# Optimization experiments

Measured on AMD Instinct MI355X. Metric: run time of the kernel, lower is better.

The kernel has to match this reference:

```python
import jax, jax.numpy as jnp
import numpy as np

N = 50000
E = 800000
IN_DIM, HID, OUT = 64, 256, 128


def gcn_conv(x, edge_index, W, b):
    """PyG GCNConv with add_self_loops=False, sym normalization, unit edge weights.
    Transform-then-propagate: out[i] = sum_{e: col[e]=i} norm[e] * (x @ W)[row[e]] + b
    norm[e] = deg^-1/2[row] * deg^-1/2[col], deg = in-degree at col.
    """
    n = x.shape[0]
    row, col = edge_index[0], edge_index[1]
    xw = x @ W  # [N, out]
    deg = jax.ops.segment_sum(jnp.ones(row.shape[0], dtype=x.dtype), col, num_segments=n)
    dis = jnp.where(deg > 0, jax.lax.rsqrt(jnp.where(deg > 0, deg, 1.0)), 0.0)
    norm = dis[row] * dis[col]  # [E]
    msg = xw[row] * norm[:, None]  # [E, out]
    out = jax.ops.segment_sum(msg, col, num_segments=n)
    return out + b


def setup_inputs() -> dict:
    key = jax.random.key(0)
    ks = jax.random.split(key, 16)
    def lin(k, fi, fo):
        s = 1.0 / np.sqrt(fi)
        k1, k2 = jax.random.split(k)
        return (jax.random.uniform(k1, (fi, fo), jnp.float32, -s, s),
                jax.random.uniform(k2, (fo,), jnp.float32, -s, s))
    x = jax.random.normal(ks[0], (N, IN_DIM), jnp.float32)
    edge_index = jax.random.randint(ks[1], (2, E), 0, N, dtype=jnp.int64)
    w_fc, b_fc = lin(ks[2], IN_DIM, HID)
    w_conv1, b_conv1 = lin(ks[3], IN_DIM, HID)
    w_fc1, b_fc1 = lin(ks[4], 2 * HID, OUT)
    w_conv2, b_conv2 = lin(ks[5], 2 * HID, OUT)
    w_fc2, b_fc2 = lin(ks[6], OUT, 1)
    w_conv3, b_conv3 = lin(ks[7], OUT, 1)
    return dict(x=x, edge_index=edge_index,
                w_fc=w_fc, b_fc=b_fc, w_conv1=w_conv1, b_conv1=b_conv1,
                w_fc1=w_fc1, b_fc1=b_fc1, w_conv2=w_conv2, b_conv2=b_conv2,
                w_fc2=w_fc2, b_fc2=b_fc2, w_conv3=w_conv3, b_conv3=b_conv3)


def reference(x, edge_index, w_fc, b_fc, w_conv1, b_conv1, w_fc1, b_fc1,
              w_conv2, b_conv2, w_fc2, b_fc2, w_conv3, b_conv3):
    # MTGCL gcn_mlp, eval mode (dropout / dropout_adj are identity)
    x1 = jax.nn.relu(x @ w_fc + b_fc)                       # [N, HID]
    x2 = jax.nn.relu(gcn_conv(x, edge_index, w_conv1, b_conv1))  # [N, HID]
    x3 = jnp.concatenate((x1, x2), axis=1)                  # [N, 2*HID]
    x5 = jax.nn.relu(x3 @ w_fc1 + b_fc1)                    # [N, OUT]
    x6 = jax.nn.relu(gcn_conv(x3, edge_index, w_conv2, b_conv2))
    x7 = x5 + x6                                            # [N, OUT]
    pre = (x7 @ w_fc2 + b_fc2) + gcn_conv(x7, edge_index, w_conv3, b_conv3)
    return pre  # [N, 1]
```

## Files before the change

kernel.cpp:

```cpp
#include <hip/hip_runtime.h>
#include <hip/hip_bf16.h>

typedef __attribute__((ext_vector_type(8))) short short8;
typedef __attribute__((ext_vector_type(4))) float f32x4;

__device__ __forceinline__ ushort bf16_bits(float v) {
    __hip_bfloat16 h = __float2bfloat16(v);
    return *reinterpret_cast<ushort*>(&h);
}
__device__ __forceinline__ float bf16_val(float v) {
    __hip_bfloat16 h = __float2bfloat16(v);
    return __bfloat162float(h);
}
__device__ __forceinline__ float bfu_lo(uint u) {
    uint t = u << 16; return __uint_as_float(t);
}
__device__ __forceinline__ float bfu_hi(uint u) {
    uint t = u & 0xffff0000u; return __uint_as_float(t);
}


__global__ __launch_bounds__(256) void k_bcount(const int* __restrict__ col,
                                                int* __restrict__ bcnt, int E) {
    __shared__ int hist[196];
    int tid = threadIdx.x;
    int base = blockIdx.x * 2048;
    if (tid < 196) hist[tid] = 0;
    __syncthreads();
    #pragma unroll
    for (int i = 0; i < 8; i++) {
        int e = base + i * 256 + tid;
        if (e < E) atomicAdd(&hist[col[e] >> 8], 1);
    }
    __syncthreads();
    if (tid < 196 && hist[tid] > 0) atomicAdd(&bcnt[tid], hist[tid]);
}

__global__ __launch_bounds__(256) void k_bscan(const int* __restrict__ bcnt,
                                               int* __restrict__ bbase,
                                               int* __restrict__ bcur, int E) {
    int i = threadIdx.x;
    int v = (i < 196) ? bcnt[i] : 0;
    int lane = i & 63, w = i >> 6;
    int s = v;
    #pragma unroll
    for (int o = 1; o < 64; o <<= 1) {
        int t = __shfl_up(s, o);
        if (lane >= o) s += t;
    }
    __shared__ int wsum[4];
    if (lane == 63) wsum[w] = s;
    __syncthreads();
    int add = 0;
    for (int ww = 0; ww < w; ww++) add += wsum[ww];
    int excl = s + add - v;
    if (i < 196) {
        bbase[i] = excl;
        bcur[i] = excl;
    }
    if (i == 195) bbase[196] = excl + v;
}

__global__ __launch_bounds__(256) void k_binA(const int* __restrict__ row,
                                              const int* __restrict__ col,
                                              int* __restrict__ bcur,
                                              uint* __restrict__ stage, int E) {
    __shared__ uint colbuf[2048];
    __shared__ int hist[196];
    __shared__ int lcur[196];
    int tid = threadIdx.x;
    int base = blockIdx.x * 2048;
    if (tid < 196) hist[tid] = 0;
    __syncthreads();
    #pragma unroll
    for (int i = 0; i < 8; i++) {
        int e = base + i * 256 + tid;
        uint c = 0xFFFFFFFFu;
        if (e < E) {
            c = (uint)col[e];
            atomicAdd(&hist[c >> 8], 1);
        }
        colbuf[i * 256 + tid] = c;
    }
    __syncthreads();
    if (tid < 196 && hist[tid] > 0) lcur[tid] = atomicAdd(&bcur[tid], hist[tid]);
    __syncthreads();
    #pragma unroll
    for (int i = 0; i < 8; i++) {
        int idx = i * 256 + tid;
        uint c = colbuf[idx];
        if (c != 0xFFFFFFFFu) {
            uint r = (uint)row[base + idx];
            int p = atomicAdd(&lcur[c >> 8], 1);
            stage[p] = (c << 16) | r;
        }
    }
}

__global__ __launch_bounds__(256) void k_binB(const uint* __restrict__ stage,
                                              const int* __restrict__ bbase,
                                              int* __restrict__ rowptr,
                                              float* __restrict__ dis,
                                              ushort* __restrict__ csr16,
                                              int n, int E) {
    __shared__ int cnt[256];
    __shared__ int cur[256];
    __shared__ int wsum[4];
    int b = blockIdx.x;
    int lo = b << 8;
    int tid = threadIdx.x;
    int gstart = bbase[b], gend = bbase[b + 1];
    cnt[tid] = 0;
    __syncthreads();
    for (int idx = gstart + tid; idx < gend; idx += 256)
        atomicAdd(&cnt[(stage[idx] >> 16) & 255], 1);
    __syncthreads();
    int v = cnt[tid];
    int lane = tid & 63, w = tid >> 6;
    int s = v;
    #pragma unroll
    for (int o = 1; o < 64; o <<= 1) {
        int t = __shfl_up(s, o);
        if (lane >= o) s += t;
    }
    if (lane == 63) wsum[w] = s;
    __syncthreads();
    int add = 0;
    for (int ww = 0; ww < w; ww++) add += wsum[ww];
    int excl = s + add - v + gstart;
    int node = lo + tid;
    if (node < n) {
        rowptr[node] = excl;
        dis[node] = v > 0 ? rsqrtf((float)v) : 0.f;
    }
    cur[tid] = excl;
    if (tid == 0 && b == gridDim.x - 1) rowptr[n] = E;
    __syncthreads();
    for (int idx = gstart + tid; idx < gend; idx += 256) {
        uint pk = stage[idx];
        int p = atomicAdd(&cur[(pk >> 16) & 255], 1);
        csr16[p] = (ushort)(pk & 0xffffu);
    }
}


__global__ __launch_bounds__(256) void k_prepX(const float* __restrict__ x,
                                               const float* __restrict__ dis,
                                               ushort* __restrict__ xh,
                                               ushort* __restrict__ xs, int total4) {
    int i = blockIdx.x * 256 + threadIdx.x;
    if (i >= total4) return;
    float4 v = reinterpret_cast<const float4*>(x)[i];
    float dn = dis[i >> 4];
    float vv[4] = {v.x, v.y, v.z, v.w};
    uint hv[2], sv[2];
    #pragma unroll
    for (int g = 0; g < 2; g++) {
        float a0 = vv[g * 2], a1 = vv[g * 2 + 1];
        hv[g] = (uint)bf16_bits(a0) | ((uint)bf16_bits(a1) << 16);
        sv[g] = (uint)bf16_bits(a0 * dn) | ((uint)bf16_bits(a1 * dn) << 16);
    }
    reinterpret_cast<uint2*>(xh)[i] = make_uint2(hv[0], hv[1]);
    reinterpret_cast<uint2*>(xs)[i] = make_uint2(sv[0], sv[1]);
}


__global__ __launch_bounds__(256) void k_agg64_csr(const ushort* __restrict__ xs,
                                                   const int* __restrict__ rowptr,
                                                   const ushort* __restrict__ csr16,
                                                   const float* __restrict__ dis,
                                                   ushort* __restrict__ agghi, int n) {
    int node = blockIdx.x * 4 + (threadIdx.x >> 6);
    if (node >= n) return;
    int lane = threadIdx.x & 63;
    int sub = lane >> 3;
    int li  = lane & 7;
    int s = rowptr[node], t = rowptr[node + 1];
    float acc[8] = {};
    int p = s;
    for (; p + 16 <= t; p += 16) {
        int rr[2];
        #pragma unroll
        for (int u = 0; u < 2; u++) rr[u] = csr16[p + u * 8 + sub];
        uint4 v[2];
        #pragma unroll
        for (int u = 0; u < 2; u++)
            v[u] = *reinterpret_cast<const uint4*>(&xs[(size_t)rr[u] * 64 + li * 8]);
        #pragma unroll
        for (int u = 0; u < 2; u++) {
            acc[0] += bfu_lo(v[u].x); acc[1] += bfu_hi(v[u].x);
            acc[2] += bfu_lo(v[u].y); acc[3] += bfu_hi(v[u].y);
            acc[4] += bfu_lo(v[u].z); acc[5] += bfu_hi(v[u].z);
            acc[6] += bfu_lo(v[u].w); acc[7] += bfu_hi(v[u].w);
        }
    }
    for (; p < t; p += 8) {
        int e = p + sub;
        if (e < t) {
            int rr = csr16[e];
            uint4 v = *reinterpret_cast<const uint4*>(&xs[(size_t)rr * 64 + li * 8]);
            acc[0] += bfu_lo(v.x); acc[1] += bfu_hi(v.x);
            acc[2] += bfu_lo(v.y); acc[3] += bfu_hi(v.y);
            acc[4] += bfu_lo(v.z); acc[5] += bfu_hi(v.z);
            acc[6] += bfu_lo(v.w); acc[7] += bfu_hi(v.w);
        }
    }
    #pragma unroll
    for (int j = 0; j < 8; j++) {
        acc[j] += __shfl_xor(acc[j], 8);
        acc[j] += __shfl_xor(acc[j], 16);
        acc[j] += __shfl_xor(acc[j], 32);
    }
    if (sub == 0) {
        float dn = dis[node];
        uint hp[4];
        #pragma unroll
        for (int g = 0; g < 4; g++) {
            float a0 = acc[g * 2] * dn, a1 = acc[g * 2 + 1] * dn;
            hp[g] = (uint)bf16_bits(a0) | ((uint)bf16_bits(a1) << 16);
        }
        *reinterpret_cast<uint4*>(&agghi[(size_t)node * 64 + li * 8]) =
            make_uint4(hp[0], hp[1], hp[2], hp[3]);
    }
}

__global__ __launch_bounds__(256) void k_agg128_x7dot(
    const ushort* __restrict__ xw,
    const int* __restrict__ rowptr,
    const ushort* __restrict__ csr16,
    const float* __restrict__ dis,
    const float* __restrict__ b2,
    const ushort* __restrict__ x5,
    const float* __restrict__ wfc2, const float* __restrict__ bfc2,
    const float* __restrict__ wc3,  const float* __restrict__ bc3,
    float* __restrict__ out, float* __restrict__ xw3, int n) {
    int node = blockIdx.x * 4 + (threadIdx.x >> 6);
    if (node >= n) return;
    int lane = threadIdx.x & 63;
    int sub = lane >> 4;
    int li  = lane & 15;
    int s = rowptr[node], t = rowptr[node + 1];
    float acc[8] = {};
    int p = s;
    for (; p + 16 <= t; p += 16) {
        int rr[4];
        #pragma unroll
        for (int u = 0; u < 4; u++) rr[u] = csr16[p + u * 4 + sub];
        uint4 v[4];
        #pragma unroll
        for (int u = 0; u < 4; u++)
            v[u] = *reinterpret_cast<const uint4*>(&xw[(size_t)rr[u] * 128 + li * 8]);
        #pragma unroll
        for (int u = 0; u < 4; u++) {
            acc[0] += bfu_lo(v[u].x); acc[1] += bfu_hi(v[u].x);
            acc[2] += bfu_lo(v[u].y); acc[3] += bfu_hi(v[u].y);
            acc[4] += bfu_lo(v[u].z); acc[5] += bfu_hi(v[u].z);
            acc[6] += bfu_lo(v[u].w); acc[7] += bfu_hi(v[u].w);
        }
    }
    for (; p < t; p += 4) {
        int e = p + sub;
        if (e < t) {
            int rr = csr16[e];
            uint4 v = *reinterpret_cast<const uint4*>(&xw[(size_t)rr * 128 + li * 8]);
            acc[0] += bfu_lo(v.x); acc[1] += bfu_hi(v.x);
            acc[2] += bfu_lo(v.y); acc[3] += bfu_hi(v.y);
            acc[4] += bfu_lo(v.z); acc[5] += bfu_hi(v.z);
            acc[6] += bfu_lo(v.w); acc[7] += bfu_hi(v.w);
        }
    }
    #pragma unroll
    for (int j = 0; j < 8; j++) {
        acc[j] += __shfl_xor(acc[j], 16);
        acc[j] += __shfl_xor(acc[j], 32);
    }
    float dn = dis[node];
    float s1 = 0.f, s2 = 0.f;
    if (sub == 0) {
        uint4 xv = *reinterpret_cast<const uint4*>(&x5[(size_t)node * 128 + li * 8]);
        float xr[8] = {bfu_lo(xv.x), bfu_hi(xv.x), bfu_lo(xv.y), bfu_hi(xv.y),
                       bfu_lo(xv.z), bfu_hi(xv.z), bfu_lo(xv.w), bfu_hi(xv.w)};
        #pragma unroll
        for (int j = 0; j < 8; j++) {
            int d = li * 8 + j;
            float x7 = xr[j] + fmaxf(dn * acc[j] + b2[d], 0.f);
            s1 += x7 * wfc2[d];
            s2 += x7 * wc3[d];
        }
    }
    #pragma unroll
    for (int o = 32; o > 0; o >>= 1) {
        s1 += __shfl_down(s1, o);
        s2 += __shfl_down(s2, o);
    }
    if (lane == 0) {
        out[node] = s1 + bfc2[0] + bc3[0];
        xw3[node] = s2 * dn;
    }
}

__global__ __launch_bounds__(256) void k_agg1_csr(const float* __restrict__ sv,
                                                  const int* __restrict__ rowptr,
                                                  const ushort* __restrict__ csr16,
                                                  const float* __restrict__ dis,
                                                  float* __restrict__ out, int n) {
    int i = blockIdx.x * 256 + threadIdx.x;
    if (i >= n) return;
    int s = rowptr[i], t = rowptr[i + 1];
    float a = 0.f;
    #pragma unroll 4
    for (int p = s; p < t; ++p) a += sv[csr16[p]];
    out[i] += dis[i] * a;
}

__global__ __launch_bounds__(256) void k_prepW(const float* __restrict__ w0,
                                               const float* __restrict__ w1,
                                               const float* __restrict__ wf1,
                                               const float* __restrict__ wf2,
                                               ushort* __restrict__ W0f,
                                               ushort* __restrict__ W1f,
                                               ushort* __restrict__ Bf) {
    int id = blockIdx.x * 256 + threadIdx.x;
    if (id < 8192) {
        int mat = id >> 12;
        int rem = id & 4095;
        int lane = rem & 63;
        int nt = (rem >> 6) & 15;
        int k0i = (rem >> 10) & 1;
        int arr = rem >> 11;
        const float* w = mat ? w1 : w0;
        ushort* dst = mat ? W1f : W0f;
        int n = nt * 16 + (lane & 15);
        int kb = k0i * 32 + (lane >> 4) * 8;
        ushort o[8];
        #pragma unroll
        for (int j = 0; j < 8; j++) {
            float v = w[(size_t)(kb + j) * 256 + n];
            o[j] = arr ? bf16_bits(v - bf16_val(v)) : bf16_bits(v);
        }
        *reinterpret_cast<int4*>(&dst[(size_t)rem * 8]) = *reinterpret_cast<const int4*>(o);
    } else if (id < 24576) {
        int rem = id - 8192;
        int lane = rem & 63;
        int nt   = (rem >> 6) & 15;
        int k0i  = (rem >> 10) & 15;
        int n = nt * 16 + (lane & 15);
        int kbase = k0i * 32 + (lane >> 4) * 8;
        ushort outv[8];
        #pragma unroll
        for (int j = 0; j < 8; j++) {
            int k = kbase + j;
            float v = (n < 128) ? wf1[(size_t)k * 128 + n]
                                : wf2[(size_t)k * 128 + (n - 128)];
            outv[j] = bf16_bits(v);
        }
        *reinterpret_cast<int4*>(&Bf[(size_t)rem * 8]) = *reinterpret_cast<const int4*>(outv);
    }
}

__device__ __forceinline__ int x3_swz(int inner) {
    return inner ^ ((((inner >> 6) & 1) << 4) ^ (((inner >> 7) & 1) << 3));
}

__global__ __launch_bounds__(256) void k_mmfused(
    const ushort* __restrict__ xh, const ushort* __restrict__ ah_,
    const ushort* __restrict__ W0f, const ushort* __restrict__ W1f,
    const float* __restrict__ b0, const float* __restrict__ b1,
    const ushort* __restrict__ Bf, const float* __restrict__ bias1,
    const float* __restrict__ dis,
    ushort* __restrict__ C1, ushort* __restrict__ C2, int M) {
    __shared__ ushort x3[4 * 16 * 512];

    const int t = threadIdx.x;
    const int lane = t & 63;
    const int wv = t >> 6;
    const int m0 = blockIdx.x * 64;
    const int ln15 = lane & 15;
    const int quad = lane >> 4;

    f32x4 acc[4][4];

    #pragma unroll
    for (int layer = 0; layer < 2; layer++) {
        const ushort* A = layer ? ah_ : xh;
        const ushort* Wf = layer ? W1f : W0f;
        const float* bias = layer ? b1 : b0;
        #pragma unroll
        for (int mt = 0; mt < 4; mt++)
            #pragma unroll
            for (int nt4 = 0; nt4 < 4; nt4++)
                acc[mt][nt4] = (f32x4){0.f, 0.f, 0.f, 0.f};

        #pragma unroll
        for (int k0i = 0; k0i < 2; k0i++) {
            short8 bh[4], bl[4];
            #pragma unroll
            for (int nt4 = 0; nt4 < 4; nt4++) {
                const ushort* pw = Wf + ((size_t)k0i * 16 + wv * 4 + nt4) * 512 + (size_t)lane * 8;
                bh[nt4] = *reinterpret_cast<const short8*>(pw);
                bl[nt4] = *reinterpret_cast<const short8*>(pw + 16384);
            }
            #pragma unroll
            for (int mt = 0; mt < 4; mt++) {
                int gm = m0 + mt * 16 + ln15;
                int gmc = gm < M - 1 ? gm : M - 1;
                size_t ia = (size_t)gmc * 64 + k0i * 32 + quad * 8;
                short8 a = *reinterpret_cast<const short8*>(&A[ia]);
                #pragma unroll
                for (int nt4 = 0; nt4 < 4; nt4++) {
                    acc[mt][nt4] = __builtin_amdgcn_mfma_f32_16x16x32_bf16(a, bh[nt4], acc[mt][nt4], 0, 0, 0);
                    acc[mt][nt4] = __builtin_amdgcn_mfma_f32_16x16x32_bf16(a, bl[nt4], acc[mt][nt4], 0, 0, 0);
                }
            }
        }

        #pragma unroll
        for (int mt = 0; mt < 4; mt++) {
            #pragma unroll
            for (int nt4 = 0; nt4 < 4; nt4++) {
                int gn = wv * 64 + nt4 * 16 + ln15;
                int gcol = gn + layer * 256;
                int k0f = gcol >> 5, qf = (gcol >> 3) & 3, j = gcol & 7;
                #pragma unroll
                for (int r = 0; r < 4; r++) {
                    int rloc = quad * 4 + r;
                    float v = fmaxf(acc[mt][nt4][r] + bias[gn], 0.f);
                    int inner = x3_swz((qf * 16 + rloc) * 8 + j);
                    x3[(mt * 16 + k0f) * 512 + inner] = bf16_bits(v);
                }
            }
        }
    }
    __syncthreads();

    #pragma unroll
    for (int mt = 0; mt < 4; mt++)
        #pragma unroll
        for (int nt = 0; nt < 4; nt++)
            acc[mt][nt] = (f32x4){0.f, 0.f, 0.f, 0.f};

    const int innerA = x3_swz(lane * 8);
    const ushort* bPtr = Bf + ((size_t)wv * 4) * 512 + (size_t)lane * 8;

    short8 bC[4];
    #pragma unroll
    for (int nt = 0; nt < 4; nt++)
        bC[nt] = *reinterpret_cast<const short8*>(bPtr + (size_t)nt * 512);

    for (int k0 = 0; k0 < 16; k0++) {
        short8 bN[4];
        if (k0 < 15) {
            #pragma unroll
            for (int nt = 0; nt < 4; nt++)
                bN[nt] = *reinterpret_cast<const short8*>(bPtr + ((size_t)(k0 + 1) * 16 + nt) * 512);
        }
        short8 aF[4];
        #pragma unroll
        for (int mt = 0; mt < 4; mt++)
            aF[mt] = *reinterpret_cast<const short8*>(&x3[(mt * 16 + k0) * 512 + innerA]);
        #pragma unroll
        for (int mt = 0; mt < 4; mt++)
            #pragma unroll
            for (int nt = 0; nt < 4; nt++)
                acc[mt][nt] = __builtin_amdgcn_mfma_f32_16x16x32_bf16(aF[mt], bC[nt], acc[mt][nt], 0, 0, 0);
        if (k0 < 15) {
            #pragma unroll
            for (int nt = 0; nt < 4; nt++) bC[nt] = bN[nt];
        }
    }

    #pragma unroll
    for (int mt = 0; mt < 4; mt++) {
        float dn[4];
        #pragma unroll
        for (int r = 0; r < 4; r++) {
            int gm = m0 + mt * 16 + quad * 4 + r;
            dn[r] = (gm < M) ? dis[gm] : 0.f;
        }
        #pragma unroll
        for (int nt = 0; nt < 4; nt++) {
            int gn = wv * 64 + nt * 16 + ln15;
            #pragma unroll
            for (int r = 0; r < 4; r++) {
                int gm = m0 + mt * 16 + quad * 4 + r;
                if (gm >= M) continue;
                float v = acc[mt][nt][r];
                if (gn < 128) {
                    C1[(size_t)gm * 128 + gn] = bf16_bits(fmaxf(v + bias1[gn], 0.f));
                } else {
                    C2[(size_t)gm * 128 + (gn - 128)] = bf16_bits(v * dn[r]);
                }
            }
        }
    }
}

extern "C" void kernel_launch(void* const* d_in, const int* in_sizes, int n_in,
                              void* d_out, int out_size, void* d_ws, size_t ws_size,
                              hipStream_t stream) {
    const float* x       = (const float*)d_in[0];
    const int*   ei      = (const int*)d_in[1];
    const float* w_fc    = (const float*)d_in[2];
    const float* b_fc    = (const float*)d_in[3];
    const float* w_conv1 = (const float*)d_in[4];
    const float* b_conv1 = (const float*)d_in[5];
    const float* w_fc1   = (const float*)d_in[6];
    const float* b_fc1   = (const float*)d_in[7];
    const float* w_conv2 = (const float*)d_in[8];
    const float* b_conv2 = (const float*)d_in[9];
    const float* w_fc2   = (const float*)d_in[10];
    const float* b_fc2   = (const float*)d_in[11];
    const float* w_conv3 = (const float*)d_in[12];
    const float* b_conv3 = (const float*)d_in[13];

    const int N = in_sizes[0] / 64;
    const int E = in_sizes[1] / 2;
    const int* row = ei;
    const int* col = ei + E;

    const int nb = (N + 255) / 256;
    const int nblk = (N + 63) / 64;

    char* p = (char*)d_ws;
    auto alloc = [&](size_t elems) {
        void* q = p; p += ((elems + 3) & ~(size_t)3) * 4; return q;
    };
    int*    bcnt    = (int*)   alloc(200);
    int*    bbase   = (int*)   alloc(200);
    int*    bcur    = (int*)   alloc(200);
    int*    rowptr  = (int*)   alloc(N + 4);
    uint*   stage   = (uint*)  alloc(E);
    ushort* csr16   = (ushort*)alloc((size_t)E / 2);
    float*  dis     = (float*) alloc(N);
    ushort* xh      = (ushort*)alloc((size_t)N * 32);
    ushort* xs      = (ushort*)alloc((size_t)N * 32);
    ushort* agghi   = (ushort*)alloc((size_t)N * 32);
    ushort* Bf      = (ushort*)alloc(65536);
    ushort* W0f     = (ushort*)alloc(16384);
    ushort* W1f     = (ushort*)alloc(16384);
    ushort* x5      = (ushort*)alloc((size_t)N * 64);
    ushort* xw2     = (ushort*)alloc((size_t)N * 64);
    float*  xw3     = (float*) alloc(N);

    float* out = (float*)d_out;

    hipMemsetAsync(bcnt, 0, 196 * sizeof(int), stream);
    k_bcount<<<(E + 2047) / 2048, 256, 0, stream>>>(col, bcnt, E);
    k_bscan<<<1, 256, 0, stream>>>(bcnt, bbase, bcur, E);
    k_binA<<<(E + 2047) / 2048, 256, 0, stream>>>(row, col, bcur, stage, E);
    k_binB<<<nb, 256, 0, stream>>>(stage, bbase, rowptr, dis, csr16, N, E);

    k_prepX<<<(N * 16 + 255) / 256, 256, 0, stream>>>(x, dis, xh, xs, N * 16);
    k_prepW<<<24576 / 256, 256, 0, stream>>>(w_fc, w_conv1, w_fc1, w_conv2,
                                             W0f, W1f, Bf);

    k_agg64_csr<<<(N + 3) / 4, 256, 0, stream>>>(xs, rowptr, csr16, dis, agghi, N);

    k_mmfused<<<nblk, 256, 0, stream>>>(xh, agghi, W0f, W1f, b_fc, b_conv1,
                                        Bf, b_fc1, dis, x5, xw2, N);

    k_agg128_x7dot<<<(N + 3) / 4, 256, 0, stream>>>(
        xw2, rowptr, csr16, dis, b_conv2, x5,
        w_fc2, b_fc2, w_conv3, b_conv3, out, xw3, N);

    k_agg1_csr<<<(N + 255) / 256, 256, 0, stream>>>(xw3, rowptr, csr16, dis, out, N);
}
```

Baseline: 250.2 us.

## Use 8 waves per block in fused matmul and stage output through LDS

The fused MLP/GCN matmul block grows from 4 to 8 wavefronts, and each wave now covers 32 output columns instead of 64. This halves per-wave accumulator registers and may raise occupancy. The final outputs are written into the shared x3 buffer with an XOR swizzle, then copied to C1/C2 as coalesced 16-byte stores instead of scattered 2-byte stores. The cost is two extra barriers and redundant A-fragment loads across more waves.

```diff
diff --git a/kernel.cpp b/kernel.cpp
--- a/kernel.cpp
+++ b/kernel.cpp
@@ -362,7 +362,7 @@
     return inner ^ ((((inner >> 6) & 1) << 4) ^ (((inner >> 7) & 1) << 3));
 }
 
-__global__ __launch_bounds__(256) void k_mmfused(
+__global__ __launch_bounds__(512) void k_mmfused(
     const ushort* __restrict__ xh, const ushort* __restrict__ ah_,
     const ushort* __restrict__ W0f, const ushort* __restrict__ W1f,
     const float* __restrict__ b0, const float* __restrict__ b1,
@@ -378,7 +378,7 @@
     const int ln15 = lane & 15;
     const int quad = lane >> 4;
 
-    f32x4 acc[4][4];
+    f32x4 acc[4][2];
 
     #pragma unroll
     for (int layer = 0; layer < 2; layer++) {
@@ -388,17 +388,17 @@
         #pragma unroll
         for (int mt = 0; mt < 4; mt++)
             #pragma unroll
-            for (int nt4 = 0; nt4 < 4; nt4++)
-                acc[mt][nt4] = (f32x4){0.f, 0.f, 0.f, 0.f};
+            for (int ntl = 0; ntl < 2; ntl++)
+                acc[mt][ntl] = (f32x4){0.f, 0.f, 0.f, 0.f};
 
         #pragma unroll
         for (int k0i = 0; k0i < 2; k0i++) {
-            short8 bh[4], bl[4];
-            #pragma unroll
-            for (int nt4 = 0; nt4 < 4; nt4++) {
-                const ushort* pw = Wf + ((size_t)k0i * 16 + wv * 4 + nt4) * 512 + (size_t)lane * 8;
-                bh[nt4] = *reinterpret_cast<const short8*>(pw);
-                bl[nt4] = *reinterpret_cast<const short8*>(pw + 16384);
+            short8 bh[2], bl[2];
+            #pragma unroll
+            for (int ntl = 0; ntl < 2; ntl++) {
+                const ushort* pw = Wf + ((size_t)k0i * 16 + wv * 2 + ntl) * 512 + (size_t)lane * 8;
+                bh[ntl] = *reinterpret_cast<const short8*>(pw);
+                bl[ntl] = *reinterpret_cast<const short8*>(pw + 16384);
             }
             #pragma unroll
             for (int mt = 0; mt < 4; mt++) {
@@ -407,24 +407,25 @@
                 size_t ia = (size_t)gmc * 64 + k0i * 32 + quad * 8;
                 short8 a = *reinterpret_cast<const short8*>(&A[ia]);
                 #pragma unroll
-                for (int nt4 = 0; nt4 < 4; nt4++) {
-                    acc[mt][nt4] = __builtin_amdgcn_mfma_f32_16x16x32_bf16(a, bh[nt4], acc[mt][nt4], 0, 0, 0);
-                    acc[mt][nt4] = __builtin_amdgcn_mfma_f32_16x16x32_bf16(a, bl[nt4], acc[mt][nt4], 0, 0, 0);
-                }
+                for (int ntl = 0; ntl < 2; ntl++)
+                    acc[mt][ntl] = __builtin_amdgcn_mfma_f32_16x16x32_bf16(a, bh[ntl], acc[mt][ntl], 0, 0, 0);
+                #pragma unroll
+                for (int ntl = 0; ntl < 2; ntl++)
+                    acc[mt][ntl] = __builtin_amdgcn_mfma_f32_16x16x32_bf16(a, bl[ntl], acc[mt][ntl], 0, 0, 0);
             }
         }
 
         #pragma unroll
         for (int mt = 0; mt < 4; mt++) {
             #pragma unroll
-            for (int nt4 = 0; nt4 < 4; nt4++) {
-                int gn = wv * 64 + nt4 * 16 + ln15;
+            for (int ntl = 0; ntl < 2; ntl++) {
+                int gn = (wv * 2 + ntl) * 16 + ln15;
                 int gcol = gn + layer * 256;
                 int k0f = gcol >> 5, qf = (gcol >> 3) & 3, j = gcol & 7;
                 #pragma unroll
                 for (int r = 0; r < 4; r++) {
                     int rloc = quad * 4 + r;
-                    float v = fmaxf(acc[mt][nt4][r] + bias[gn], 0.f);
+                    float v = fmaxf(acc[mt][ntl][r] + bias[gn], 0.f);
                     int inner = x3_swz((qf * 16 + rloc) * 8 + j);
                     x3[(mt * 16 + k0f) * 512 + inner] = bf16_bits(v);
                 }
@@ -436,23 +437,23 @@
     #pragma unroll
     for (int mt = 0; mt < 4; mt++)
         #pragma unroll
-        for (int nt = 0; nt < 4; nt++)
-            acc[mt][nt] = (f32x4){0.f, 0.f, 0.f, 0.f};
+        for (int ntl = 0; ntl < 2; ntl++)
+            acc[mt][ntl] = (f32x4){0.f, 0.f, 0.f, 0.f};
 
     const int innerA = x3_swz(lane * 8);
-    const ushort* bPtr = Bf + ((size_t)wv * 4) * 512 + (size_t)lane * 8;
-
-    short8 bC[4];
-    #pragma unroll
-    for (int nt = 0; nt < 4; nt++)
-        bC[nt] = *reinterpret_cast<const short8*>(bPtr + (size_t)nt * 512);
+    const ushort* bPtr = Bf + ((size_t)wv * 2) * 512 + (size_t)lane * 8;
+
+    short8 bC[2];
+    #pragma unroll
+    for (int ntl = 0; ntl < 2; ntl++)
+        bC[ntl] = *reinterpret_cast<const short8*>(bPtr + (size_t)ntl * 512);
 
     for (int k0 = 0; k0 < 16; k0++) {
-        short8 bN[4];
+        short8 bN[2];
         if (k0 < 15) {
             #pragma unroll
-            for (int nt = 0; nt < 4; nt++)
-                bN[nt] = *reinterpret_cast<const short8*>(bPtr + ((size_t)(k0 + 1) * 16 + nt) * 512);
+            for (int ntl = 0; ntl < 2; ntl++)
+                bN[ntl] = *reinterpret_cast<const short8*>(bPtr + ((size_t)(k0 + 1) * 16 + ntl) * 512);
         }
         short8 aF[4];
         #pragma unroll
@@ -461,13 +462,14 @@
         #pragma unroll
         for (int mt = 0; mt < 4; mt++)
             #pragma unroll
-            for (int nt = 0; nt < 4; nt++)
-                acc[mt][nt] = __builtin_amdgcn_mfma_f32_16x16x32_bf16(aF[mt], bC[nt], acc[mt][nt], 0, 0, 0);
+            for (int ntl = 0; ntl < 2; ntl++)
+                acc[mt][ntl] = __builtin_amdgcn_mfma_f32_16x16x32_bf16(aF[mt], bC[ntl], acc[mt][ntl], 0, 0, 0);
         if (k0 < 15) {
             #pragma unroll
-            for (int nt = 0; nt < 4; nt++) bC[nt] = bN[nt];
-        }
-    }
+            for (int ntl = 0; ntl < 2; ntl++) bC[ntl] = bN[ntl];
+        }
+    }
+    __syncthreads();
 
     #pragma unroll
     for (int mt = 0; mt < 4; mt++) {
@@ -478,19 +480,35 @@
             dn[r] = (gm < M) ? dis[gm] : 0.f;
         }
         #pragma unroll
-        for (int nt = 0; nt < 4; nt++) {
-            int gn = wv * 64 + nt * 16 + ln15;
+        for (int ntl = 0; ntl < 2; ntl++) {
+            int gn = (wv * 2 + ntl) * 16 + ln15;
             #pragma unroll
             for (int r = 0; r < 4; r++) {
-                int gm = m0 + mt * 16 + quad * 4 + r;
-                if (gm >= M) continue;
-                float v = acc[mt][nt][r];
-                if (gn < 128) {
-                    C1[(size_t)gm * 128 + gn] = bf16_bits(fmaxf(v + bias1[gn], 0.f));
-                } else {
-                    C2[(size_t)gm * 128 + (gn - 128)] = bf16_bits(v * dn[r]);
-                }
+                int row64 = mt * 16 + quad * 4 + r;
+                float v = acc[mt][ntl][r];
+                ushort ov = (gn < 128) ? bf16_bits(fmaxf(v + bias1[gn], 0.f))
+                                       : bf16_bits(v * dn[r]);
+                int idx = row64 * 256 + gn;
+                idx ^= ((row64 >> 2) & 3) << 4;
+                x3[idx] = ov;
             }
+        }
+    }
+    __syncthreads();
+
+    #pragma unroll
+    for (int c = 0; c < 4; c++) {
+        int offu = c * 4096 + t * 8;
+        int row64 = offu >> 8;
+        int colu = offu & 255;
+        int src = row64 * 256 + (colu ^ (((row64 >> 2) & 3) << 4));
+        uint4 v = *reinterpret_cast<const uint4*>(&x3[src]);
+        int gm = m0 + row64;
+        if (gm < M) {
+            if (colu < 128)
+                *reinterpret_cast<uint4*>(&C1[(size_t)gm * 128 + colu]) = v;
+            else
+                *reinterpret_cast<uint4*>(&C2[(size_t)gm * 128 + (colu - 128)]) = v;
         }
     }
 }
@@ -556,7 +574,7 @@
 
     k_agg64_csr<<<(N + 3) / 4, 256, 0, stream>>>(xs, rowptr, csr16, dis, agghi, N);
 
-    k_mmfused<<<nblk, 256, 0, stream>>>(xh, agghi, W0f, W1f, b_fc, b_conv1,
+    k_mmfused<<<nblk, 512, 0, stream>>>(xh, agghi, W0f, W1f, b_fc, b_conv1,
                                         Bf, b_fc1, dis, x5, xw2, N);
 
     k_agg128_x7dot<<<(N + 3) / 4, 256, 0, stream>>>(
```

Measured after the change: 244.6 us. -2.2%, faster.
